# Kernel optimization log

Measured on AMD Instinct MI355X. Metric: run time of the kernel, lower is better.

Reference implementation:

```python
import jax, jax.numpy as jnp
import numpy as np

BINS = [16]*20 + [32]*10 + [64]*5 + [65]  # sum = 1025, K = 36 bands
EMBED_DIM = 128
MAX_F = 2 * max(BINS)  # padded feature width = 130
EPS = 1e-5


def setup_inputs() -> dict:
    key = jax.random.key(0)
    ks = jax.random.split(key, 5)
    B, NB, T = 8, sum(BINS), 2048
    K = len(BINS)
    spec_ri = jax.random.normal(ks[0], (B, NB, T, 2), dtype=jnp.float32)
    # Per-band params, padded to MAX_F along the feature axis.
    gamma = jnp.ones((K, MAX_F), dtype=jnp.float32)
    beta = jnp.zeros((K, MAX_F), dtype=jnp.float32)
    W = jax.random.normal(ks[1], (K, EMBED_DIM, MAX_F), dtype=jnp.float32) * 0.05
    b = jax.random.normal(ks[2], (K, EMBED_DIM), dtype=jnp.float32) * 0.01
    return {"spec_ri": spec_ri, "gamma": gamma, "beta": beta, "W": W, "b": b}


def reference(spec_ri, gamma, beta, W, b):
    # spec_ri: (B, n_bins, T, 2) real/imag pair == torch.view_as_real(complex input)
    B, _, T, _ = spec_ri.shape
    outs = []
    start = 0
    for k, nb in enumerate(BINS):
        f = 2 * nb
        xb = spec_ri[:, start:start + nb]          # (B, nb, T, 2)
        start += nb
        # permute(0,2,1,3) then flatten -> interleaved [re0, im0, re1, im1, ...]
        x = jnp.transpose(xb, (0, 2, 1, 3)).reshape(B, T, f)  # (B, T, 2*nb)
        mu = jnp.mean(x, axis=-1, keepdims=True)
        var = jnp.mean(jnp.square(x - mu), axis=-1, keepdims=True)
        xn = (x - mu) / jnp.sqrt(var + EPS) * gamma[k, :f] + beta[k, :f]
        y = jnp.einsum('btf,ef->bte', xn, W[k, :, :f]) + b[k]  # (B, T, E)
        outs.append(jnp.transpose(y, (0, 2, 1)))   # (B, E, T)
    return jnp.stack(outs, axis=-2)                 # (B, E, K, T)
```

## Files before the change

### kernel.cpp

```cpp
#include <hip/hip_runtime.h>
#include <stdint.h>

#define T_FULL 2048
#define TT 128
#define NB_TOT 1025
#define KBANDS 36
#define EMBED 128
#define MAXF 130
#define FPAD 160
#define EPSV 1e-5f
#define LDS_W 84

typedef __attribute__((ext_vector_type(8))) short short8;
typedef __attribute__((ext_vector_type(4))) float floatx4;
typedef __attribute__((ext_vector_type(2))) float floatx2;

__device__ __forceinline__ void band_info(int band, int& nb, int& start) {
  if (band < 20)      { nb = 16; start = band << 4; }
  else if (band < 30) { nb = 32; start = 320 + ((band - 20) << 5); }
  else if (band < 35) { nb = 64; start = 640 + ((band - 30) << 6); }
  else                { nb = 65; start = 960; }
}

__device__ __forceinline__ unsigned short f2bf(float x) {
  union { float f; uint32_t u; } c; c.f = x;
  return (unsigned short)((c.u + 0x7FFFu + ((c.u >> 16) & 1u)) >> 16);
}

__global__ void __launch_bounds__(256) prep_kernel(
    const float* __restrict__ W, const float* __restrict__ gamma,
    const float* __restrict__ beta, const float* __restrict__ bvec,
    unsigned short* __restrict__ Wg, float* __restrict__ S, float* __restrict__ BB)
{
  int k = blockIdx.x;
  int w = threadIdx.x >> 6, lane = threadIdx.x & 63;
  int e = blockIdx.y * 4 + w;
  int nb, start; band_info(k, nb, start);
  int f = nb * 2;
  const float* wrow = W + ((size_t)k * EMBED + e) * MAXF;
  const float* grow = gamma + (size_t)k * MAXF;
  const float* brow = beta + (size_t)k * MAXF;
  unsigned short* orow = Wg + ((size_t)k * EMBED + e) * FPAD;

  float bb = 0.f;
  int i1 = lane, i2 = lane + 64, i3 = lane + 128;
  float v1 = 0.f, v2 = 0.f, v3 = 0.f;
  if (i1 < f) { float wv = wrow[i1]; v1 = wv * grow[i1]; bb += wv * brow[i1]; }
  if (i2 < f) { float wv = wrow[i2]; v2 = wv * grow[i2]; bb += wv * brow[i2]; }
  if (i3 < f) { float wv = wrow[i3]; v3 = wv * grow[i3]; bb += wv * brow[i3]; }
  orow[i1] = f2bf(v1);
  orow[i2] = f2bf(v2);
  if (i3 < FPAD) orow[i3] = f2bf(v3);
  float s = v1 + v2 + v3;
  #pragma unroll
  for (int off = 32; off > 0; off >>= 1) {
    s  += __shfl_down(s, off);
    bb += __shfl_down(bb, off);
  }
  if (lane == 0) {
    S[k * EMBED + e]  = s;
    BB[k * EMBED + e] = bvec[k * EMBED + e] + bb;
  }
}

__global__ void __launch_bounds__(256, 3) band_kernel(
    const float* __restrict__ spec, const unsigned short* __restrict__ Wg,
    const float* __restrict__ S, const float* __restrict__ BB,
    float* __restrict__ out)
{
  __shared__ uint32_t xn[TT * LDS_W];
  __shared__ float part_s[4][64];
  __shared__ float part_q[4][64];
  __shared__ float mu_l[TT];
  __shared__ float rs_l[TT];

  int tid = threadIdx.x;
  int w = tid >> 6, lane = tid & 63;
  int band = blockIdx.y, b = blockIdx.z;
  int t0 = blockIdx.x * TT;
  int nb, start; band_info(band, nb, start);
  int f = nb * 2;
  int ksteps = (f + 31) >> 5;

  int tl = ((w & 1) << 6) | lane;
  int swz = (tl >> 3) & 3;
  const floatx2* sp = (const floatx2*)spec +
      ((size_t)(b * NB_TOT + start) * T_FULL + (t0 + tl));
  float s = 0.f, q = 0.f;
  for (int j = (w >> 1); j < nb; j += 2) {
    floatx2 v = sp[(size_t)j * T_FULL];
    float re = v.x, im = v.y;
    s += re + im;
    q += re * re + im * im;
    xn[tl * LDS_W + (j ^ (swz << 2))] =
        (uint32_t)f2bf(re) | ((uint32_t)f2bf(im) << 16);
  }
  if (f & 31) {
    for (int idx = tid; idx < TT * 15; idx += 256) {
      int t = idx / 15, jz = 65 + idx % 15;
      xn[t * LDS_W + (jz ^ (((t >> 3) & 3) << 2))] = 0;
    }
  }
  part_s[w][lane] = s;
  part_q[w][lane] = q;
  __syncthreads();
  if (tid < TT) {
    int h = tid >> 6, li = tid & 63;
    float su = part_s[h][li] + part_s[h + 2][li];
    float sq = part_q[h][li] + part_q[h + 2][li];
    float inv_f = 1.0f / (float)f;
    float mu = su * inv_f;
    float var = sq * inv_f - mu * mu;
    mu_l[tid] = mu;
    rs_l[tid] = rsqrtf(var + EPSV);
  }
  __syncthreads();

  int lane16 = lane & 15, quad = lane >> 4;
  floatx4 acc[2][8];
  #pragma unroll
  for (int i = 0; i < 2; ++i)
    #pragma unroll
    for (int j = 0; j < 8; ++j) acc[i][j] = floatx4{0.f, 0.f, 0.f, 0.f};

  int ebase = w * 32;
  const unsigned short* wgb = Wg + ((size_t)band * EMBED + ebase) * FPAD;
  for (int kk = 0; kk < ksteps; ++kk) {
    short8 a0 = *(const short8*)(wgb + (size_t)lane16 * FPAD + kk * 32 + quad * 8);
    short8 a1 = *(const short8*)(wgb + (size_t)(16 + lane16) * FPAD + kk * 32 + quad * 8);
    #pragma unroll
    for (int nt = 0; nt < 8; ++nt) {
      int t = nt * 16 + lane16;
      int blk = kk * 4 + (quad ^ ((t >> 3) & 3));
      short8 bfr = *(const short8*)&xn[t * LDS_W + blk * 4];
      acc[0][nt] = __builtin_amdgcn_mfma_f32_16x16x32_bf16(a0, bfr, acc[0][nt], 0, 0, 0);
      acc[1][nt] = __builtin_amdgcn_mfma_f32_16x16x32_bf16(a1, bfr, acc[1][nt], 0, 0, 0);
    }
  }

  float muv[8], rsv[8];
  #pragma unroll
  for (int nt = 0; nt < 8; ++nt) {
    int t = nt * 16 + lane16;
    muv[nt] = mu_l[t];
    rsv[nt] = rs_l[t];
  }
  int obase = ((b * EMBED) * KBANDS + band) * T_FULL + t0;
  const float* Sb = S + band * EMBED + ebase;
  const float* Bb = BB + band * EMBED + ebase;
  #pragma unroll
  for (int et = 0; et < 2; ++et) {
    int e0 = et * 16 + quad * 4;
    floatx4 Sv = *(const floatx4*)(Sb + e0);
    floatx4 Bv = *(const floatx4*)(Bb + e0);
    #pragma unroll
    for (int nt = 0; nt < 8; ++nt) {
      int t = nt * 16 + lane16;
      #pragma unroll
      for (int r = 0; r < 4; ++r) {
        float y = rsv[nt] * (acc[et][nt][r] - muv[nt] * Sv[r]) + Bv[r];
        out[(size_t)obase + (size_t)(ebase + e0 + r) * (KBANDS * T_FULL) + t] = y;
      }
    }
  }
}

extern "C" void kernel_launch(void* const* d_in, const int* in_sizes, int n_in,
                              void* d_out, int out_size, void* d_ws, size_t ws_size,
                              hipStream_t stream) {
  const float* spec  = (const float*)d_in[0];
  const float* gamma = (const float*)d_in[1];
  const float* beta  = (const float*)d_in[2];
  const float* W     = (const float*)d_in[3];
  const float* bvec  = (const float*)d_in[4];
  float* out = (float*)d_out;

  unsigned short* Wg = (unsigned short*)d_ws;
  size_t wg_bytes = (size_t)KBANDS * EMBED * FPAD * sizeof(unsigned short);
  float* S  = (float*)((char*)d_ws + wg_bytes);
  float* BB = S + KBANDS * EMBED;

  prep_kernel<<<dim3(KBANDS, 32), dim3(256), 0, stream>>>(W, gamma, beta, bvec, Wg, S, BB);
  band_kernel<<<dim3(T_FULL / TT, KBANDS, 8), dim3(256), 0, stream>>>(spec, Wg, S, BB, out);
}
```

Baseline: 462.9 us.

## Specialize band kernel per band size and vectorize output stores via swapped MFMA operands

Templates the band kernel on bins-per-band, LDS row width, k-steps and occupancy, and launches four specialized grids so loops are fully unrolled and LDS is sized per band group. The MFMA operand order is swapped so each lane holds four consecutive time steps, which allows 16-byte vector stores to the output instead of scalar strided stores. The bf16 conversion is simplified to round-half-up bit arithmetic. This adds launch overhead from four kernels and small rounding differences.

```diff
diff --git a/kernel.cpp b/kernel.cpp
--- a/kernel.cpp
+++ b/kernel.cpp
@@ -9,7 +9,6 @@
 #define MAXF 130
 #define FPAD 160
 #define EPSV 1e-5f
-#define LDS_W 84
 
 typedef __attribute__((ext_vector_type(8))) short short8;
 typedef __attribute__((ext_vector_type(4))) float floatx4;
@@ -63,42 +62,46 @@
   }
 }
 
-__global__ void __launch_bounds__(256, 3) band_kernel(
+template<int NBB, int LDSW, int KSTEPS, bool FILL, int MINW>
+__global__ void __launch_bounds__(256, MINW) band_kernel(
     const float* __restrict__ spec, const unsigned short* __restrict__ Wg,
     const float* __restrict__ S, const float* __restrict__ BB,
-    float* __restrict__ out)
+    float* __restrict__ out, int band0, int start0)
 {
-  __shared__ uint32_t xn[TT * LDS_W];
+  __shared__ uint32_t xn[TT * LDSW];
   __shared__ float part_s[4][64];
   __shared__ float part_q[4][64];
-  __shared__ float mu_l[TT];
-  __shared__ float rs_l[TT];
+  __shared__ __align__(16) float mu_l[TT];
+  __shared__ __align__(16) float rs_l[TT];
 
   int tid = threadIdx.x;
   int w = tid >> 6, lane = tid & 63;
-  int band = blockIdx.y, b = blockIdx.z;
+  int band = band0 + blockIdx.y, b = blockIdx.z;
+  int start = start0 + blockIdx.y * NBB;
   int t0 = blockIdx.x * TT;
-  int nb, start; band_info(band, nb, start);
-  int f = nb * 2;
-  int ksteps = (f + 31) >> 5;
 
   int tl = ((w & 1) << 6) | lane;
-  int swz = (tl >> 3) & 3;
+  uint32_t swz = ((tl >> 3) & 3) << 2;
   const floatx2* sp = (const floatx2*)spec +
       ((size_t)(b * NB_TOT + start) * T_FULL + (t0 + tl));
   float s = 0.f, q = 0.f;
-  for (int j = (w >> 1); j < nb; j += 2) {
+  #pragma unroll
+  for (int j = (w >> 1); j < NBB; j += 2) {
     floatx2 v = sp[(size_t)j * T_FULL];
     float re = v.x, im = v.y;
     s += re + im;
     q += re * re + im * im;
-    xn[tl * LDS_W + (j ^ (swz << 2))] =
-        (uint32_t)f2bf(re) | ((uint32_t)f2bf(im) << 16);
+    uint32_t ure, uim;
+    __builtin_memcpy(&ure, &re, 4);
+    __builtin_memcpy(&uim, &im, 4);
+    uint32_t pk = ((ure + 0x8000u) >> 16) | (((uim + 0x8000u) >> 16) << 16);
+    xn[tl * LDSW + (j ^ swz)] = pk;
   }
-  if (f & 31) {
-    for (int idx = tid; idx < TT * 15; idx += 256) {
-      int t = idx / 15, jz = 65 + idx % 15;
-      xn[t * LDS_W + (jz ^ (((t >> 3) & 3) << 2))] = 0;
+  if (FILL) {
+    const int TW = KSTEPS * 16 - NBB;
+    for (int idx = tid; idx < TT * TW; idx += 256) {
+      int t = idx / TW, jz = NBB + idx % TW;
+      xn[t * LDSW + (jz ^ (((t >> 3) & 3) << 2))] = 0;
     }
   }
   part_s[w][lane] = s;
@@ -108,7 +111,7 @@
     int h = tid >> 6, li = tid & 63;
     float su = part_s[h][li] + part_s[h + 2][li];
     float sq = part_q[h][li] + part_q[h + 2][li];
-    float inv_f = 1.0f / (float)f;
+    const float inv_f = 1.0f / (float)(2 * NBB);
     float mu = su * inv_f;
     float var = sq * inv_f - mu * mu;
     mu_l[tid] = mu;
@@ -125,43 +128,38 @@
 
   int ebase = w * 32;
   const unsigned short* wgb = Wg + ((size_t)band * EMBED + ebase) * FPAD;
-  for (int kk = 0; kk < ksteps; ++kk) {
-    short8 a0 = *(const short8*)(wgb + (size_t)lane16 * FPAD + kk * 32 + quad * 8);
-    short8 a1 = *(const short8*)(wgb + (size_t)(16 + lane16) * FPAD + kk * 32 + quad * 8);
+  #pragma unroll
+  for (int kk = 0; kk < KSTEPS; ++kk) {
+    short8 b0 = *(const short8*)(wgb + (size_t)lane16 * FPAD + kk * 32 + quad * 8);
+    short8 b1 = *(const short8*)(wgb + (size_t)(16 + lane16) * FPAD + kk * 32 + quad * 8);
     #pragma unroll
     for (int nt = 0; nt < 8; ++nt) {
       int t = nt * 16 + lane16;
       int blk = kk * 4 + (quad ^ ((t >> 3) & 3));
-      short8 bfr = *(const short8*)&xn[t * LDS_W + blk * 4];
-      acc[0][nt] = __builtin_amdgcn_mfma_f32_16x16x32_bf16(a0, bfr, acc[0][nt], 0, 0, 0);
-      acc[1][nt] = __builtin_amdgcn_mfma_f32_16x16x32_bf16(a1, bfr, acc[1][nt], 0, 0, 0);
+      short8 afr = *(const short8*)&xn[t * LDSW + blk * 4];
+      acc[0][nt] = __builtin_amdgcn_mfma_f32_16x16x32_bf16(afr, b0, acc[0][nt], 0, 0, 0);
+      acc[1][nt] = __builtin_amdgcn_mfma_f32_16x16x32_bf16(afr, b1, acc[1][nt], 0, 0, 0);
     }
   }
 
-  float muv[8], rsv[8];
+  int e_lo = ebase + lane16;
+  const size_t row_stride = (size_t)KBANDS * T_FULL;
+  float S0 = S[band * EMBED + e_lo],  S1 = S[band * EMBED + e_lo + 16];
+  float B0 = BB[band * EMBED + e_lo], B1 = BB[band * EMBED + e_lo + 16];
+  float* o0 = out + ((size_t)(b * EMBED + e_lo) * KBANDS + band) * T_FULL + t0 + quad * 4;
+  float* o1 = o0 + 16 * row_stride;
   #pragma unroll
   for (int nt = 0; nt < 8; ++nt) {
-    int t = nt * 16 + lane16;
-    muv[nt] = mu_l[t];
-    rsv[nt] = rs_l[t];
-  }
-  int obase = ((b * EMBED) * KBANDS + band) * T_FULL + t0;
-  const float* Sb = S + band * EMBED + ebase;
-  const float* Bb = BB + band * EMBED + ebase;
-  #pragma unroll
-  for (int et = 0; et < 2; ++et) {
-    int e0 = et * 16 + quad * 4;
-    floatx4 Sv = *(const floatx4*)(Sb + e0);
-    floatx4 Bv = *(const floatx4*)(Bb + e0);
+    floatx4 mu4 = *(const floatx4*)&mu_l[nt * 16 + quad * 4];
+    floatx4 rs4 = *(const floatx4*)&rs_l[nt * 16 + quad * 4];
+    floatx4 y0, y1;
     #pragma unroll
-    for (int nt = 0; nt < 8; ++nt) {
-      int t = nt * 16 + lane16;
-      #pragma unroll
-      for (int r = 0; r < 4; ++r) {
-        float y = rsv[nt] * (acc[et][nt][r] - muv[nt] * Sv[r]) + Bv[r];
-        out[(size_t)obase + (size_t)(ebase + e0 + r) * (KBANDS * T_FULL) + t] = y;
-      }
+    for (int r = 0; r < 4; ++r) {
+      y0[r] = rs4[r] * (acc[0][nt][r] - mu4[r] * S0) + B0;
+      y1[r] = rs4[r] * (acc[1][nt][r] - mu4[r] * S1) + B1;
     }
+    *(floatx4*)(o0 + nt * 16) = y0;
+    *(floatx4*)(o1 + nt * 16) = y1;
   }
 }
 
@@ -181,5 +179,12 @@
   float* BB = S + KBANDS * EMBED;
 
   prep_kernel<<<dim3(KBANDS, 32), dim3(256), 0, stream>>>(W, gamma, beta, bvec, Wg, S, BB);
-  band_kernel<<<dim3(T_FULL / TT, KBANDS, 8), dim3(256), 0, stream>>>(spec, Wg, S, BB, out);
+  band_kernel<16, 20, 1, false, 4><<<dim3(T_FULL / TT, 20, 8), dim3(256), 0, stream>>>(
+      spec, Wg, S, BB, out, 0, 0);
+  band_kernel<32, 36, 2, false, 4><<<dim3(T_FULL / TT, 10, 8), dim3(256), 0, stream>>>(
+      spec, Wg, S, BB, out, 20, 320);
+  band_kernel<64, 84, 4, false, 3><<<dim3(T_FULL / TT, 5, 8), dim3(256), 0, stream>>>(
+      spec, Wg, S, BB, out, 30, 640);
+  band_kernel<65, 84, 5, true, 3><<<dim3(T_FULL / TT, 1, 8), dim3(256), 0, stream>>>(
+      spec, Wg, S, BB, out, 35, 960);
 }
```

After: 472.2 us. 2.0% more time.
